# Kernel tuning notes

Hardware: AMD Instinct MI355X
Metric: run time of the kernel (lower is better)

Reference implementation:

```python
import jax, jax.numpy as jnp
import numpy as np

N_BINS = 1024
GAMMA = 0.99
BETA = 0.25
MIN_ASSIGN = 0.1 / N_BINS  # self.min_assignment
INITIAL_PATIENCE = 10.0


def setup_inputs() -> dict:
    key = jax.random.key(0)
    ks = jax.random.split(key, 5)
    N, d_x, d_z = 262144, 64, 32
    return {
        "x": jax.random.normal(ks[0], (N, d_x), jnp.float32),
        "W_enc": jax.random.normal(ks[1], (d_x, d_z), jnp.float32) / np.sqrt(d_x).astype(np.float32),
        "b_enc": jnp.zeros((d_z,), jnp.float32),
        "vectors": jax.random.normal(ks[2], (N_BINS, d_z), jnp.float32),
        "W_dec": jax.random.normal(ks[3], (d_z, d_x), jnp.float32) / np.sqrt(d_z).astype(np.float32),
        "b_dec": jnp.zeros((d_x,), jnp.float32),
        "assignments": jnp.full((N_BINS,), INITIAL_PATIENCE, jnp.float32),
        "noise": jax.random.normal(ks[4], (N_BINS, d_z), jnp.float32) * 1e-5,
    }


def _gauss_logprob(mu, x):
    # unit-variance Gaussian, summed over last (event) dim -> shape x.shape[:-1]
    d = x.shape[-1]
    return -0.5 * (jnp.sum((x - mu) ** 2, axis=-1) + d * jnp.log(2.0 * jnp.pi).astype(x.dtype))


def reference(x, W_enc, b_enc, vectors, W_dec, b_dec, assignments, noise):
    # ----- encoder + codebook nearest-neighbor lookup -----
    z = x @ W_enc + b_enc  # [N, d_z]
    # squared L2 distances to all codes: [N, n_bins]
    d2 = (jnp.sum(z * z, axis=-1, keepdims=True)
          - 2.0 * (z @ vectors.T)
          + jnp.sum(vectors * vectors, axis=-1)[None, :])
    idx = jnp.argmin(d2, axis=-1)          # [N]
    quantized = vectors[idx]               # [N, d_z]
    z_q = z + jax.lax.stop_gradient(quantized - z)  # straight-through

    # ----- reconstruction (Gaussian decoder) + commitment -----
    mu = z_q @ W_dec + b_dec
    reconstruction_loss = -jnp.mean(_gauss_logprob(mu, x))
    commitment_loss = jnp.mean((jax.lax.stop_gradient(quantized) - z) ** 2)
    loss = reconstruction_loss + BETA * commitment_loss

    # ----- training-mode buffer updates (EMA + dead-code reinit) -----
    N = idx.shape[0]
    # one_hot.mean(0) without materializing [N, n_bins]
    counts = jax.ops.segment_sum(jnp.ones((N,), jnp.float32), idx, num_segments=N_BINS)
    batch_assign = counts / N                                   # [n_bins]
    assign_ema = GAMMA * assignments + (1.0 - GAMMA) * batch_assign
    # (one_hot[:,:,None] * z[:,None,:]).sum(0) == per-bin sum of z
    sum_z = jax.ops.segment_sum(jax.lax.stop_gradient(z), idx, num_segments=N_BINS)
    mean_vector = sum_z / (batch_assign[:, None] * N)           # may be nan where count==0 (masked below)

    not_assigned = assign_ema * N < MIN_ASSIGN                  # [n_bins] bool
    max_idx = jnp.argmax(batch_assign)                          # constant through the loop (as in torch)

    def step(carry, i):
        vecs, a = carry
        do = not_assigned[i]
        new_a = a[max_idx] / 2.0
        vecs = vecs.at[i].set(jnp.where(do, vecs[max_idx] + noise[i], vecs[i]))
        a = a.at[i].set(jnp.where(do, new_a, a[i]))
        a = a.at[max_idx].set(jnp.where(do, new_a, a[max_idx]))
        return (vecs, a), None

    # torch pops from the end of the not-assigned list -> iterate high->low index
    (vecs2, assign_ema), _ = jax.lax.scan(step, (vectors, assign_ema),
                                          jnp.arange(N_BINS - 1, -1, -1))

    mean_vector = jnp.where(batch_assign[:, None] == 0.0, vecs2, mean_vector)
    new_vectors = GAMMA * vecs2 + (1.0 - GAMMA) * mean_vector
    return loss, new_vectors, assign_ema
```

## Files before the change

kernel.cpp:

```cpp
#include <hip/hip_runtime.h>
#include <math.h>

#define N_ROWS 262144
#define DX 64
#define DZ 32
#define NB 1024
#define NBF 262144.0f
#define MIN_ASSIGN (0.1f / 1024.0f)
#define BIAS 512.0f

typedef short shortx8 __attribute__((ext_vector_type(8)));
typedef float floatx4 __attribute__((ext_vector_type(4)));
typedef float floatx2 __attribute__((ext_vector_type(2)));

#define WS_RECON  0
#define WS_COMMIT 1
#define WS_VNORMB 64
#define WS_MUNORM 1088
#define WS_WENCT  2112
#define WS_WDECB  3136
#define WS_VBF    4160
#define WS_VBF2   20544
#define WS_ZP     36928
#define WS_BIDX   4231232
#define WS_SUMZC  4362304
#define WS_COUNTS 4395072
#define WS_PART   4396096
#define WS_FINS   6558784
#define WS_RPART  6559872
#define WS_CPART  6563968
#define WS_TOTAL  6568064
#define PART_STRIDE 33792
#define HCHUNKS 64
#define HROWS  (N_ROWS / HCHUNKS)
#define HROLES 17
#define HBLOCKS (HROLES * HCHUNKS)
#define HSCALE 2048.0f
#define RF_BLOCKS 132
#define ENC_THREADS 128
#define ENC_BLOCKS (N_ROWS / ENC_THREADS)

#define XSTR 68
#define ZSTR 40
#define YSTR 36
#define SMEM_ZBF  0
#define SMEM_YBF  10240
#define SMEM_XBF  0
#define SMEM_SKEY 19456
#define SMEM_SZ   19968

#define FB_RECON  0
#define FB_COMMIT 1
#define FB_COUNTS 64
#define FB_SUMZ   1088
#define FB_VNORM  33856
#define FB_MUTAB  34880
#define FB_ZERO_N 33856

static __device__ __forceinline__ short f2bf(float f) {
    union { float f; unsigned u; } v; v.f = f;
    unsigned r = v.u + 0x7FFFu + ((v.u >> 16) & 1u);
    return (short)(r >> 16);
}
static __device__ __forceinline__ float bits2f(unsigned u) {
    union { unsigned u; float f; } v; v.u = u; return v.f;
}

__global__ __launch_bounds__(256) void zero_kernel(float* __restrict__ p, int n) {
    int i = blockIdx.x * 256 + threadIdx.x;
    if (i < n) p[i] = 0.0f;
}

__global__ __launch_bounds__(64) void vq_prep(
    const float* __restrict__ vectors, const float* __restrict__ W_enc,
    const float* __restrict__ W_dec, const float* __restrict__ b_dec,
    float* __restrict__ ws)
{
    const int j = blockIdx.x;
    const int t = threadIdx.x;
    float* vnormb = ws + WS_VNORMB;
    float* munorm = ws + WS_MUNORM;
    short* vbf  = (short*)(ws + WS_VBF);
    short* vbf2 = (short*)(ws + WS_VBF2);
    short* wencT = (short*)(ws + WS_WENCT);
    short* wdecb = (short*)(ws + WS_WDECB);

    if (j == 0 && t == 2) ws[WS_FINS + 2] = 0.0f;
    if (j == 0) {
        #pragma unroll
        for (int c = 0; c < DZ; ++c)
            wencT[c * DX + t] = f2bf(W_enc[t * DZ + c]);
    }
    if (j == 1) {
        #pragma unroll
        for (int c = 0; c < DZ; ++c)
            wdecb[c * DX + t] = f2bf(W_dec[c * DX + t]);
    }

    __shared__ float v[DZ];
    if (t < DZ) {
        float vv = vectors[j * DZ + t];
        v[t] = vv;
        vbf[j * DZ + t]  = f2bf(vv);
        vbf2[j * DZ + t] = f2bf(-2.0f * vv);
    }
    __syncthreads();
    float m = b_dec[t];
    #pragma unroll
    for (int k = 0; k < DZ; ++k) m = fmaf(v[k], W_dec[k * DX + t], m);
    float ms = m * m;
    #pragma unroll
    for (int off = 32; off > 0; off >>= 1) ms += __shfl_down(ms, off, 64);
    if (t == 0) {
        munorm[j] = ms;
        float s = 0.0f;
        #pragma unroll
        for (int k = 0; k < DZ; ++k) s = fmaf(v[k], v[k], s);
        vnormb[j] = s + BIAS;
    }
}

__global__ __launch_bounds__(ENC_THREADS, 4) void vq_encmin(
    const float* __restrict__ x, const short* __restrict__ wencT,
    const float* __restrict__ b_enc, const short* __restrict__ wdecb,
    const float* __restrict__ b_dec, const short* __restrict__ vbf,
    const short* __restrict__ vbf2, const float* __restrict__ vnormb,
    const float* __restrict__ munorm,
    unsigned* __restrict__ zp, unsigned short* __restrict__ bidx_out,
    float* __restrict__ rpart, float* __restrict__ cpart)
{
    __shared__ __attribute__((aligned(16))) char smem[SMEM_SZ];
    short* xbf = (short*)(smem + SMEM_XBF);
    short* zbf = (short*)(smem + SMEM_ZBF);
    short* ybf = (short*)(smem + SMEM_YBF);
    unsigned* skey = (unsigned*)(smem + SMEM_SKEY);

    const int t = threadIdx.x;
    const int r = blockIdx.x * ENC_THREADS + t;

    const float4* xsrc = (const float4*)(x + (size_t)blockIdx.x * ENC_THREADS * DX);
    #pragma unroll
    for (int i = 0; i < 16; ++i) {
        float4 v = xsrc[i * ENC_THREADS + t];
        unsigned a0 = __builtin_bit_cast(unsigned, v.x) + 0x8000u;
        unsigned a1 = __builtin_bit_cast(unsigned, v.y) + 0x8000u;
        unsigned a2 = __builtin_bit_cast(unsigned, v.z) + 0x8000u;
        unsigned a3 = __builtin_bit_cast(unsigned, v.w) + 0x8000u;
        uint2 pv;
        pv.x = __builtin_amdgcn_perm(a1, a0, 0x07060302u);
        pv.y = __builtin_amdgcn_perm(a3, a2, 0x07060302u);
        const int e = i * ENC_THREADS + t;
        *(uint2*)&xbf[(e >> 4) * XSTR + (e & 15) * 4] = pv;
    }
    __syncthreads();

    float xnorm = 0.0f, xb = 0.0f;
    #pragma unroll
    for (int i = 0; i < 16; ++i) {
        uint2 q = *(const uint2*)&xbf[t * XSTR + i * 4];
        const float4 bd = ((const float4*)b_dec)[i];
        float f0 = bits2f(q.x << 16), f1 = bits2f(q.x & 0xFFFF0000u);
        float f2 = bits2f(q.y << 16), f3 = bits2f(q.y & 0xFFFF0000u);
        xnorm = fmaf(f0, f0, xnorm); xnorm = fmaf(f1, f1, xnorm);
        xnorm = fmaf(f2, f2, xnorm); xnorm = fmaf(f3, f3, xnorm);
        xb = fmaf(f0, bd.x, xb); xb = fmaf(f1, bd.y, xb);
        xb = fmaf(f2, bd.z, xb); xb = fmaf(f3, bd.w, xb);
    }

    const int w = t >> 6, l = t & 63, lm = l & 15, lq4 = l >> 4;
    shortx8 we[2][2], wd[2][2];
    #pragma unroll
    for (int ct = 0; ct < 2; ++ct)
        #pragma unroll
        for (int kk = 0; kk < 2; ++kk) {
            we[ct][kk] = *(const shortx8*)&wencT[(ct * 16 + lm) * DX + kk * 32 + lq4 * 8];
            wd[ct][kk] = *(const shortx8*)&wdecb[(ct * 16 + lm) * DX + kk * 32 + lq4 * 8];
        }
    const float be0 = b_enc[lm], be1 = b_enc[16 + lm];

    unsigned zpkv[16], ypkv[16];
    #pragma unroll
    for (int rt = 0; rt < 4; ++rt) {
        const int arow = (w * 64 + rt * 16 + lm) * XSTR;
        union { uint2 q[2]; shortx8 s; } a0u, a1u;
        a0u.q[0] = *(const uint2*)&xbf[arow + lq4 * 8];
        a0u.q[1] = *(const uint2*)&xbf[arow + lq4 * 8 + 4];
        a1u.q[0] = *(const uint2*)&xbf[arow + 32 + lq4 * 8];
        a1u.q[1] = *(const uint2*)&xbf[arow + 32 + lq4 * 8 + 4];

        floatx4 z0 = {be0, be0, be0, be0}, z1 = {be1, be1, be1, be1};
        z0 = __builtin_amdgcn_mfma_f32_16x16x32_bf16(a0u.s, we[0][0], z0, 0, 0, 0);
        z0 = __builtin_amdgcn_mfma_f32_16x16x32_bf16(a1u.s, we[0][1], z0, 0, 0, 0);
        z1 = __builtin_amdgcn_mfma_f32_16x16x32_bf16(a0u.s, we[1][0], z1, 0, 0, 0);
        z1 = __builtin_amdgcn_mfma_f32_16x16x32_bf16(a1u.s, we[1][1], z1, 0, 0, 0);
        floatx4 y0 = {0.f, 0.f, 0.f, 0.f}, y1 = {0.f, 0.f, 0.f, 0.f};
        y0 = __builtin_amdgcn_mfma_f32_16x16x32_bf16(a0u.s, wd[0][0], y0, 0, 0, 0);
        y0 = __builtin_amdgcn_mfma_f32_16x16x32_bf16(a1u.s, wd[0][1], y0, 0, 0, 0);
        y1 = __builtin_amdgcn_mfma_f32_16x16x32_bf16(a0u.s, wd[1][0], y1, 0, 0, 0);
        y1 = __builtin_amdgcn_mfma_f32_16x16x32_bf16(a1u.s, wd[1][1], y1, 0, 0, 0);

        #pragma unroll
        for (int reg = 0; reg < 4; ++reg) {
            unsigned zl = __builtin_bit_cast(unsigned, z0[reg]) + 0x8000u;
            unsigned zh = __builtin_bit_cast(unsigned, z1[reg]) + 0x8000u;
            zpkv[rt * 4 + reg] = __builtin_amdgcn_perm(zh, zl, 0x07060302u);
            unsigned yl = __builtin_bit_cast(unsigned, y0[reg]) + 0x8000u;
            unsigned yh = __builtin_bit_cast(unsigned, y1[reg]) + 0x8000u;
            ypkv[rt * 4 + reg] = __builtin_amdgcn_perm(yh, yl, 0x07060302u);
        }
    }
    __syncthreads();

    #pragma unroll
    for (int k = 0; k < 16; ++k) {
        const int row = w * 64 + (k >> 2) * 16 + lq4 * 4 + (k & 3);
        zbf[row * ZSTR + lm]      = (short)(zpkv[k] & 0xFFFFu);
        zbf[row * ZSTR + 16 + lm] = (short)(zpkv[k] >> 16);
        ybf[row * YSTR + lm]      = (short)(ypkv[k] & 0xFFFFu);
        ybf[row * YSTR + 16 + lm] = (short)(ypkv[k] >> 16);
    }
    __syncthreads();

    shortx8 afrag[4];
    #pragma unroll
    for (int rt = 0; rt < 4; ++rt)
        afrag[rt] = *(const shortx8*)&zbf[(w * 64 + rt * 16 + lm) * ZSTR + lq4 * 8];

    unsigned key[16];
    #pragma unroll
    for (int k = 0; k < 16; ++k) key[k] = 0xFFFFFFFFu;

    #pragma unroll 8
    for (int jt = 0; jt < 64; ++jt) {
        const int jbase = jt * 16 + lm;
        const shortx8 bfrag = *(const shortx8*)&vbf2[(size_t)jbase * DZ + lq4 * 8];
        const float vn = vnormb[jbase];
        floatx4 cin = {vn, vn, vn, vn};
        #pragma unroll
        for (int rt = 0; rt < 4; ++rt) {
            floatx4 acc = __builtin_amdgcn_mfma_f32_16x16x32_bf16(
                afrag[rt], bfrag, cin, 0, 0, 0);
            #pragma unroll
            for (int reg = 0; reg < 4; ++reg) {
                unsigned u = __builtin_bit_cast(unsigned, acc[reg]);
                unsigned pk = (u & 0xFFFFFC00u) | (unsigned)jbase;
                int k = rt * 4 + reg;
                key[k] = key[k] < pk ? key[k] : pk;
            }
        }
    }

    #pragma unroll
    for (int k = 0; k < 16; ++k) {
        unsigned kv = key[k];
        #pragma unroll
        for (int m = 1; m <= 8; m <<= 1) {
            unsigned ov = __shfl_xor(kv, m, 64);
            kv = ov < kv ? ov : kv;
        }
        if (lm == 0)
            skey[w * 64 + (k >> 2) * 16 + lq4 * 4 + (k & 3)] = kv;
    }
    __syncthreads();

    const unsigned kr = skey[t];
    const int bsel = (int)(kr & 1023u);
    const float score = bits2f(kr & 0xFFFFFC00u);
    bidx_out[r] = (unsigned short)bsel;

    float znorm = 0.0f;
    #pragma unroll
    for (int i = 0; i < 4; ++i) {
        uint4 q = *(const uint4*)&zbf[t * ZSTR + i * 8];
        zp[(size_t)(4 * i + 0) * N_ROWS + r] = q.x;
        zp[(size_t)(4 * i + 1) * N_ROWS + r] = q.y;
        zp[(size_t)(4 * i + 2) * N_ROWS + r] = q.z;
        zp[(size_t)(4 * i + 3) * N_ROWS + r] = q.w;
        float f0 = bits2f(q.x << 16), f1 = bits2f(q.x & 0xFFFF0000u);
        float f2 = bits2f(q.y << 16), f3 = bits2f(q.y & 0xFFFF0000u);
        float f4 = bits2f(q.z << 16), f5 = bits2f(q.z & 0xFFFF0000u);
        float f6 = bits2f(q.w << 16), f7 = bits2f(q.w & 0xFFFF0000u);
        znorm = fmaf(f0, f0, znorm); znorm = fmaf(f1, f1, znorm);
        znorm = fmaf(f2, f2, znorm); znorm = fmaf(f3, f3, znorm);
        znorm = fmaf(f4, f4, znorm); znorm = fmaf(f5, f5, znorm);
        znorm = fmaf(f6, f6, znorm); znorm = fmaf(f7, f7, znorm);
    }
    float commit = znorm + (score - BIAS);

    float dot = 0.0f;
    #pragma unroll
    for (int i = 0; i < 8; ++i) {
        uint2 yq = *(const uint2*)&ybf[t * YSTR + i * 4];
        uint2 vq = *(const uint2*)&vbf[(size_t)bsel * DZ + i * 4];
        dot = fmaf(bits2f(yq.x << 16), bits2f(vq.x << 16), dot);
        dot = fmaf(bits2f(yq.x & 0xFFFF0000u), bits2f(vq.x & 0xFFFF0000u), dot);
        dot = fmaf(bits2f(yq.y << 16), bits2f(vq.y << 16), dot);
        dot = fmaf(bits2f(yq.y & 0xFFFF0000u), bits2f(vq.y & 0xFFFF0000u), dot);
    }
    float rs = xnorm - 2.0f * (dot + xb) + munorm[bsel];

    #pragma unroll
    for (int off = 32; off > 0; off >>= 1) {
        rs     += __shfl_down(rs, off, 64);
        commit += __shfl_down(commit, off, 64);
    }
    if (l == 0) {
        rpart[blockIdx.x * 2 + w] = rs;
        cpart[blockIdx.x * 2 + w] = commit;
    }
}

__global__ __launch_bounds__(256) void vq_hist(
    const unsigned* __restrict__ zp, const unsigned short* __restrict__ bidx,
    float* __restrict__ part)
{
    __shared__ int h[2 * NB];
    const int t = threadIdx.x;
    const int ci    = blockIdx.x % HROLES;
    const int chunk = blockIdx.x / HROLES;

    #pragma unroll
    for (int i = 0; i < 8; ++i) h[t + 256 * i] = 0;
    __syncthreads();

    const int base = chunk * HROWS;
    if (ci < 16) {
        const unsigned* zc = zp + (size_t)ci * N_ROWS;
        #pragma unroll 4
        for (int i = 0; i < HROWS / 256; ++i) {
            int r = base + t + 256 * i;
            unsigned w = zc[r];
            int b = bidx[r];
            atomicAdd(&h[b],      __float2int_rn(bits2f(w << 16) * HSCALE));
            atomicAdd(&h[b + NB], __float2int_rn(bits2f(w & 0xFFFF0000u) * HSCALE));
        }
        __syncthreads();
        float* pp = part + (size_t)chunk * PART_STRIDE + (size_t)(2 * ci) * NB;
        #pragma unroll
        for (int i = 0; i < 8; ++i)
            pp[t + 256 * i] = (float)h[t + 256 * i] * (1.0f / HSCALE);
    } else {
        #pragma unroll 4
        for (int i = 0; i < HROWS / 256; ++i) {
            int r = base + t + 256 * i;
            atomicAdd(&h[bidx[r]], 1);
        }
        __syncthreads();
        float* pp = part + (size_t)chunk * PART_STRIDE + (size_t)32 * NB;
        #pragma unroll
        for (int i = 0; i < 4; ++i) pp[t + 256 * i] = (float)h[t + 256 * i];
    }
}

__global__ __launch_bounds__(256) void vq_redfin(
    const float* __restrict__ part, const float* __restrict__ assignments,
    float* __restrict__ ws, float* __restrict__ out)
{
    const int t = threadIdx.x;
    {
        const int o = blockIdx.x * 256 + t;
        float s = 0.0f;
        #pragma unroll 8
        for (int c = 0; c < HCHUNKS; ++c)
            s += part[(size_t)c * PART_STRIDE + o];
        (ws + WS_SUMZC)[o] = s;
    }
    __shared__ int sdone;
    __threadfence();
    __syncthreads();
    if (t == 0) {
        unsigned old = atomicAdd((unsigned*)ws + WS_FINS + 2, 1u);
        sdone = ((old % (unsigned)RF_BLOCKS) == (unsigned)(RF_BLOCKS - 1)) ? 1 : 0;
    }
    __syncthreads();
    if (!sdone) return;
    __threadfence();

    __shared__ float h[2048];
    __shared__ float sred[4], cred[4];
    __shared__ int s_mx;
    const float* counts = ws + WS_COUNTS;

    {
        const float* rp = ws + WS_RPART;
        const float* cp = ws + WS_CPART;
        float rsum = 0.0f, csum = 0.0f;
        #pragma unroll
        for (int i = 0; i < 16; ++i) {
            rsum += rp[t + 256 * i];
            csum += cp[t + 256 * i];
        }
        #pragma unroll
        for (int off = 32; off > 0; off >>= 1) {
            rsum += __shfl_down(rsum, off, 64);
            csum += __shfl_down(csum, off, 64);
        }
        if ((t & 63) == 0) { sred[t >> 6] = rsum; cred[t >> 6] = csum; }
    }

    float* af           = h;
    unsigned char* dd   = (unsigned char*)(h + 1024);
    int*   tsum         = (int*)(h + 1280);
    float* rv           = h + 1536;
    int*   ri           = (int*)(h + 1792);

    float cnt[4]; int dloc[4];
    float bestv = -1.0f; int besti = 0;
    #pragma unroll
    for (int u = 0; u < 4; ++u) {
        int b = 4 * t + u;
        float c = counts[b]; cnt[u] = c;
        float ba = c / NBF;
        float ae = 0.99f * assignments[b] + 0.01f * ba;
        af[b] = ae;
        int d = (ae * NBF < MIN_ASSIGN) ? 1 : 0;
        dd[b] = (unsigned char)d; dloc[u] = d;
        if (ba > bestv) { bestv = ba; besti = b; }
    }
    rv[t] = bestv; ri[t] = besti;
    __syncthreads();
    for (int s = 128; s > 0; s >>= 1) {
        if (t < s) {
            float ov = rv[t + s]; int oi = ri[t + s];
            if (ov > rv[t] || (ov == rv[t] && oi < ri[t])) { rv[t] = ov; ri[t] = oi; }
        }
        __syncthreads();
    }
    if (t == 0) s_mx = ri[0];
    __syncthreads();
    const int mx = s_mx;
    const float a0mx = af[mx];
    const int na_mx = dd[mx];

    tsum[t] = dloc[0] + dloc[1] + dloc[2] + dloc[3];
    __syncthreads();
    for (int off = 1; off < 256; off <<= 1) {
        int v2 = (t + off < 256) ? tsum[t + off] : 0;
        __syncthreads();
        tsum[t] += v2;
        __syncthreads();
    }
    const int K = tsum[0];
    const int Snext = (t < 255) ? tsum[t + 1] : 0;
    int suf[4];
    suf[3] = dloc[3]; suf[2] = dloc[2] + suf[3];
    suf[1] = dloc[1] + suf[2]; suf[0] = dloc[0] + suf[1];

    #pragma unroll
    for (int u = 0; u < 4; ++u) {
        int b = 4 * t + u;
        float av = af[b];
        int rank = suf[u] + Snext;
        int isd = dd[b];
        if (isd) av = ldexpf(a0mx, -rank);
        if (b == mx && K > 0) av = ldexpf(a0mx, -K);
        out[1 + NB * DZ + b] = av;
        ws[WS_FINS + 64 + b] = (float)isd;
    }
    if (t == 0) {
        ((int*)ws)[WS_FINS] = mx;
        ws[WS_FINS + 1] = (float)na_mx;
        float rtot = sred[0] + sred[1] + sred[2] + sred[3];
        float ctot = cred[0] + cred[1] + cred[2] + cred[3];
        float recon = 0.5f * (rtot / NBF) + 32.0f * 1.8378770664093453f;
        float commit = ctot / (NBF * (float)DZ);
        out[0] = recon + 0.25f * commit;
    }
}

__global__ __launch_bounds__(256) void vq_fin_vec(
    const float* __restrict__ vectors, const float* __restrict__ noise,
    const float* __restrict__ ws, float* __restrict__ out)
{
    const int idx = blockIdx.x * 256 + threadIdx.x;
    const int b = idx >> 5, c = idx & 31;
    const int mx = ((const int*)ws)[WS_FINS];
    const float na_mx = ws[WS_FINS + 1];
    const float isd = ws[WS_FINS + 64 + b];
    const float cnt = (ws + WS_COUNTS)[b];
    const float* sumzc = ws + WS_SUMZC;

    float v2 = vectors[b * DZ + c];
    if (isd != 0.0f) {
        const float mxn = (b < mx) ? na_mx : 0.0f;
        v2 = vectors[mx * DZ + c] + mxn * noise[mx * DZ + c] + noise[b * DZ + c];
    }
    float mean = (cnt == 0.0f) ? v2 : (sumzc[(size_t)c * NB + b] / cnt);
    out[1 + b * DZ + c] = 0.99f * v2 + 0.01f * mean;
}

__global__ __launch_bounds__(64) void vq_prep_fb(
    const float* __restrict__ vectors, const float* __restrict__ W_dec,
    const float* __restrict__ b_dec, float* __restrict__ vnorm,
    float* __restrict__ mu_table)
{
    const int j = blockIdx.x;
    const int t = threadIdx.x;
    __shared__ float v[DZ];
    if (t < DZ) v[t] = vectors[j * DZ + t];
    __syncthreads();
    float m = b_dec[t];
    #pragma unroll
    for (int k = 0; k < DZ; ++k) m = fmaf(v[k], W_dec[k * DX + t], m);
    mu_table[(size_t)j * DX + t] = m;
    if (t == 0) {
        float s = 0.0f;
        #pragma unroll
        for (int k = 0; k < DZ; ++k) s = fmaf(v[k], v[k], s);
        vnorm[j] = s;
    }
}

__global__ __launch_bounds__(256) void vq_main_atomic(
    const float* __restrict__ x, const float* __restrict__ W_enc,
    const float* __restrict__ b_enc, const float* __restrict__ vectors,
    const float* __restrict__ vnorm, const float* __restrict__ mu_table,
    float* __restrict__ counts, float* __restrict__ sum_z,
    float* __restrict__ recon_acc, float* __restrict__ commit_acc)
{
    const int r = blockIdx.x * 256 + threadIdx.x;
    float xr[DX];
    const float4* xp = reinterpret_cast<const float4*>(x + (size_t)r * DX);
    #pragma unroll
    for (int i = 0; i < DX / 4; ++i) {
        float4 v = xp[i];
        xr[4 * i + 0] = v.x; xr[4 * i + 1] = v.y;
        xr[4 * i + 2] = v.z; xr[4 * i + 3] = v.w;
    }
    float z[DZ];
    #pragma unroll
    for (int c = 0; c < DZ; ++c) z[c] = b_enc[c];
    #pragma unroll
    for (int k = 0; k < DX; ++k) {
        float xk = xr[k];
        #pragma unroll
        for (int c = 0; c < DZ; ++c) z[c] = fmaf(xk, W_enc[k * DZ + c], z[c]);
    }
    float znorm = 0.0f;
    #pragma unroll
    for (int c = 0; c < DZ; ++c) znorm = fmaf(z[c], z[c], znorm);
    float zm2[DZ];
    #pragma unroll
    for (int c = 0; c < DZ; ++c) zm2[c] = -2.0f * z[c];

    float best = 3.4e38f;
    int bi = 0;
    for (int j = 0; j < NB; ++j) {
        const float* vj = vectors + j * DZ;
        float s0 = vnorm[j], s1 = 0.0f, s2 = 0.0f, s3 = 0.0f;
        #pragma unroll
        for (int c = 0; c < DZ; c += 4) {
            s0 = fmaf(zm2[c + 0], vj[c + 0], s0);
            s1 = fmaf(zm2[c + 1], vj[c + 1], s1);
            s2 = fmaf(zm2[c + 2], vj[c + 2], s2);
            s3 = fmaf(zm2[c + 3], vj[c + 3], s3);
        }
        float s = (s0 + s1) + (s2 + s3);
        if (s < best) { best = s; bi = j; }
    }
    float commit_row = znorm + best;

    float rs = 0.0f;
    const float4* mup = reinterpret_cast<const float4*>(mu_table + (size_t)bi * DX);
    #pragma unroll
    for (int i = 0; i < DX / 4; ++i) {
        float4 m = mup[i];
        float d0 = xr[4 * i + 0] - m.x; rs = fmaf(d0, d0, rs);
        float d1 = xr[4 * i + 1] - m.y; rs = fmaf(d1, d1, rs);
        float d2 = xr[4 * i + 2] - m.z; rs = fmaf(d2, d2, rs);
        float d3 = xr[4 * i + 3] - m.w; rs = fmaf(d3, d3, rs);
    }
    atomicAdd(&counts[bi], 1.0f);
    #pragma unroll
    for (int c = 0; c < DZ; ++c)
        atomicAdd(&sum_z[(size_t)bi * DZ + c], -0.5f * zm2[c]);
    #pragma unroll
    for (int off = 32; off > 0; off >>= 1) {
        rs += __shfl_down(rs, off, 64);
        commit_row += __shfl_down(commit_row, off, 64);
    }
    if ((threadIdx.x & 63) == 0) {
        atomicAdd(recon_acc, rs);
        atomicAdd(commit_acc, commit_row);
    }
}

__global__ __launch_bounds__(1024) void vq_finalize_fb(
    const float* __restrict__ vectors, const float* __restrict__ assignments,
    const float* __restrict__ noise, const float* __restrict__ counts,
    const float* __restrict__ sum_z, const float* __restrict__ recon_acc,
    const float* __restrict__ commit_acc, float* __restrict__ out)
{
    __shared__ float a[NB];
    __shared__ unsigned char na[NB];
    __shared__ float rv[NB];
    __shared__ int ri[NB];
    __shared__ int s_max_idx;
    const int t = threadIdx.x;

    const float cnt = counts[t];
    const float ba = cnt / NBF;
    const float ae = 0.99f * assignments[t] + 0.01f * ba;
    a[t] = ae;
    na[t] = (ae * NBF < MIN_ASSIGN) ? 1 : 0;
    rv[t] = ba; ri[t] = t;
    __syncthreads();
    for (int s = NB / 2; s > 0; s >>= 1) {
        if (t < s) {
            float ov = rv[t + s]; int oi = ri[t + s];
            if (ov > rv[t] || (ov == rv[t] && oi < ri[t])) { rv[t] = ov; ri[t] = oi; }
        }
        __syncthreads();
    }
    if (t == 0) s_max_idx = ri[0];
    __syncthreads();
    const int mx = s_max_idx;
    if (t == 0) {
        for (int i = NB - 1; i >= 0; --i) {
            if (na[i]) { float v = 0.5f * a[mx]; a[i] = v; a[mx] = v; }
        }
    }
    __syncthreads();
    out[1 + NB * DZ + t] = a[t];
    const bool dead = (na[t] != 0);
    #pragma unroll
    for (int c = 0; c < DZ; ++c) {
        float v2 = dead ? (vectors[mx * DZ + c] + noise[t * DZ + c])
                        : vectors[t * DZ + c];
        float mean = (cnt == 0.0f) ? v2 : (sum_z[(size_t)t * DZ + c] / cnt);
        out[1 + t * DZ + c] = 0.99f * v2 + 0.01f * mean;
    }
    if (t == 0) {
        float recon = 0.5f * (recon_acc[0] / NBF) + 32.0f * 1.8378770664093453f;
        float commit = commit_acc[0] / (NBF * (float)DZ);
        out[0] = recon + 0.25f * commit;
    }
}

extern "C" void kernel_launch(void* const* d_in, const int* in_sizes, int n_in,
                              void* d_out, int out_size, void* d_ws, size_t ws_size,
                              hipStream_t stream)
{
    const float* x           = (const float*)d_in[0];
    const float* W_enc       = (const float*)d_in[1];
    const float* b_enc       = (const float*)d_in[2];
    const float* vectors     = (const float*)d_in[3];
    const float* W_dec       = (const float*)d_in[4];
    const float* b_dec       = (const float*)d_in[5];
    const float* assignments = (const float*)d_in[6];
    const float* noise       = (const float*)d_in[7];
    float* out = (float*)d_out;
    float* ws  = (float*)d_ws;

    if (ws_size >= (size_t)WS_TOTAL * sizeof(float)) {
        vq_prep<<<NB, 64, 0, stream>>>(vectors, W_enc, W_dec, b_dec, ws);
        vq_encmin<<<ENC_BLOCKS, ENC_THREADS, 0, stream>>>(x,
            (const short*)(ws + WS_WENCT), b_enc,
            (const short*)(ws + WS_WDECB), b_dec,
            (const short*)(ws + WS_VBF), (const short*)(ws + WS_VBF2),
            ws + WS_VNORMB, ws + WS_MUNORM,
            (unsigned*)(ws + WS_ZP), (unsigned short*)(ws + WS_BIDX),
            ws + WS_RPART, ws + WS_CPART);
        vq_hist<<<HBLOCKS, 256, 0, stream>>>(
            (const unsigned*)(ws + WS_ZP),
            (const unsigned short*)(ws + WS_BIDX),
            ws + WS_PART);
        vq_redfin<<<RF_BLOCKS, 256, 0, stream>>>(
            ws + WS_PART, assignments, ws, out);
        vq_fin_vec<<<(NB * DZ) / 256, 256, 0, stream>>>(vectors, noise, ws, out);
    } else {
        zero_kernel<<<(FB_ZERO_N + 255) / 256, 256, 0, stream>>>(ws, FB_ZERO_N);
        vq_prep_fb<<<NB, 64, 0, stream>>>(vectors, W_dec, b_dec,
            ws + FB_VNORM, ws + FB_MUTAB);
        vq_main_atomic<<<N_ROWS / 256, 256, 0, stream>>>(x, W_enc, b_enc, vectors,
            ws + FB_VNORM, ws + FB_MUTAB, ws + FB_COUNTS, ws + FB_SUMZ,
            ws + FB_RECON, ws + FB_COMMIT);
        vq_finalize_fb<<<1, NB, 0, stream>>>(vectors, assignments, noise,
            ws + FB_COUNTS, ws + FB_SUMZ, ws + FB_RECON, ws + FB_COMMIT, out);
    }
}
```

Baseline: 164.2 us.

## Fuse partial reduction and finalize into histogram kernel via last-block pattern

Drops the separate reduce/finalize kernel. The last histogram block to finish (detected with an atomic counter) now reduces the count partials and runs the assignment/dead-code finalize. The per-bin sum_z reduction over chunks moves into the final vector kernel, with its thread mapping changed so bins are contiguous. This saves one launch and the SUMZC round trip, but the count reduction runs serially in a single block and output writes become strided.

```diff
diff --git a/kernel.cpp b/kernel.cpp
--- a/kernel.cpp
+++ b/kernel.cpp
@@ -36,7 +36,6 @@
 #define HROLES 17
 #define HBLOCKS (HROLES * HCHUNKS)
 #define HSCALE 2048.0f
-#define RF_BLOCKS 132
 #define ENC_THREADS 128
 #define ENC_BLOCKS (N_ROWS / ENC_THREADS)
 
@@ -312,8 +311,10 @@
 
 __global__ __launch_bounds__(256) void vq_hist(
     const unsigned* __restrict__ zp, const unsigned short* __restrict__ bidx,
-    float* __restrict__ part)
-{
+    const float* __restrict__ assignments, float* __restrict__ ws,
+    float* __restrict__ out)
+{
+    float* part = ws + WS_PART;
     __shared__ int h[2 * NB];
     const int t = threadIdx.x;
     const int ci    = blockIdx.x % HROLES;
@@ -350,37 +351,31 @@
         #pragma unroll
         for (int i = 0; i < 4; ++i) pp[t + 256 * i] = (float)h[t + 256 * i];
     }
-}
-
-__global__ __launch_bounds__(256) void vq_redfin(
-    const float* __restrict__ part, const float* __restrict__ assignments,
-    float* __restrict__ ws, float* __restrict__ out)
-{
-    const int t = threadIdx.x;
-    {
-        const int o = blockIdx.x * 256 + t;
+
+    __shared__ int sdone;
+    __threadfence();
+    __syncthreads();
+    if (t == 0) {
+        unsigned old = atomicAdd((unsigned*)ws + WS_FINS + 2, 1u);
+        sdone = ((old % (unsigned)HBLOCKS) == (unsigned)(HBLOCKS - 1)) ? 1 : 0;
+    }
+    __syncthreads();
+    if (!sdone) return;
+    __threadfence();
+
+    __shared__ float cs[NB];
+    #pragma unroll
+    for (int i = 0; i < 4; ++i) {
+        const int b = i * 256 + t;
         float s = 0.0f;
         #pragma unroll 8
         for (int c = 0; c < HCHUNKS; ++c)
-            s += part[(size_t)c * PART_STRIDE + o];
-        (ws + WS_SUMZC)[o] = s;
-    }
-    __shared__ int sdone;
-    __threadfence();
-    __syncthreads();
-    if (t == 0) {
-        unsigned old = atomicAdd((unsigned*)ws + WS_FINS + 2, 1u);
-        sdone = ((old % (unsigned)RF_BLOCKS) == (unsigned)(RF_BLOCKS - 1)) ? 1 : 0;
-    }
-    __syncthreads();
-    if (!sdone) return;
-    __threadfence();
-
-    __shared__ float h[2048];
+            s += part[(size_t)c * PART_STRIDE + (size_t)32 * NB + b];
+        cs[b] = s;
+        (ws + WS_COUNTS)[b] = s;
+    }
+
     __shared__ float sred[4], cred[4];
-    __shared__ int s_mx;
-    const float* counts = ws + WS_COUNTS;
-
     {
         const float* rp = ws + WS_RPART;
         const float* cp = ws + WS_CPART;
@@ -397,19 +392,22 @@
         }
         if ((t & 63) == 0) { sred[t >> 6] = rsum; cred[t >> 6] = csum; }
     }
-
-    float* af           = h;
-    unsigned char* dd   = (unsigned char*)(h + 1024);
-    int*   tsum         = (int*)(h + 1280);
-    float* rv           = h + 1536;
-    int*   ri           = (int*)(h + 1792);
+    __syncthreads();
+
+    __shared__ float h2[2048];
+    __shared__ int s_mx;
+    float* af           = h2;
+    unsigned char* dd   = (unsigned char*)(h2 + 1024);
+    int*   tsum         = (int*)(h2 + 1280);
+    float* rv           = h2 + 1536;
+    int*   ri           = (int*)(h2 + 1792);
 
     float cnt[4]; int dloc[4];
     float bestv = -1.0f; int besti = 0;
     #pragma unroll
     for (int u = 0; u < 4; ++u) {
         int b = 4 * t + u;
-        float c = counts[b]; cnt[u] = c;
+        float c = cs[b]; cnt[u] = c;
         float ba = c / NBF;
         float ae = 0.99f * assignments[b] + 0.01f * ba;
         af[b] = ae;
@@ -468,24 +466,31 @@
     }
 }
 
-__global__ __launch_bounds__(256) void vq_fin_vec(
+__global__ __launch_bounds__(256) void vq_finvec2(
     const float* __restrict__ vectors, const float* __restrict__ noise,
     const float* __restrict__ ws, float* __restrict__ out)
 {
     const int idx = blockIdx.x * 256 + threadIdx.x;
-    const int b = idx >> 5, c = idx & 31;
+    const int b = idx & (NB - 1);
+    const int c = idx >> 10;
+    const float* part = ws + WS_PART;
+
+    float s = 0.0f;
+    #pragma unroll 8
+    for (int ch = 0; ch < HCHUNKS; ++ch)
+        s += part[(size_t)ch * PART_STRIDE + (size_t)c * NB + b];
+
     const int mx = ((const int*)ws)[WS_FINS];
     const float na_mx = ws[WS_FINS + 1];
     const float isd = ws[WS_FINS + 64 + b];
     const float cnt = (ws + WS_COUNTS)[b];
-    const float* sumzc = ws + WS_SUMZC;
 
     float v2 = vectors[b * DZ + c];
     if (isd != 0.0f) {
         const float mxn = (b < mx) ? na_mx : 0.0f;
         v2 = vectors[mx * DZ + c] + mxn * noise[mx * DZ + c] + noise[b * DZ + c];
     }
-    float mean = (cnt == 0.0f) ? v2 : (sumzc[(size_t)c * NB + b] / cnt);
+    float mean = (cnt == 0.0f) ? v2 : (s / cnt);
     out[1 + b * DZ + c] = 0.99f * v2 + 0.01f * mean;
 }
 
@@ -664,10 +669,8 @@
         vq_hist<<<HBLOCKS, 256, 0, stream>>>(
             (const unsigned*)(ws + WS_ZP),
             (const unsigned short*)(ws + WS_BIDX),
-            ws + WS_PART);
-        vq_redfin<<<RF_BLOCKS, 256, 0, stream>>>(
-            ws + WS_PART, assignments, ws, out);
-        vq_fin_vec<<<(NB * DZ) / 256, 256, 0, stream>>>(vectors, noise, ws, out);
+            assignments, ws, out);
+        vq_finvec2<<<(NB * DZ) / 256, 256, 0, stream>>>(vectors, noise, ws, out);
     } else {
         zero_kernel<<<(FB_ZERO_N + 255) / 256, 256, 0, stream>>>(ws, FB_ZERO_N);
         vq_prep_fb<<<NB, 64, 0, stream>>>(vectors, W_dec, b_dec,
```

New measurement: 268.5 us. +63.5%, slower.

## Shrink encmin blocks to 64 rows, load x directly into MFMA fragments, drop block syncs

Applied to the files above, without the earlier changes.

The encoder/argmin kernel now handles 64 rows per block instead of 128, with 32 rows per wave. It loads x from global memory straight into MFMA A-fragments instead of staging it in shared memory, and it computes the decoder dot product per lane using shuffles. This removes the x and y shared buffers and all __syncthreads, lowers register and LDS use so occupancy can rise (launch bounds go from 4 to 8), and doubles the number of blocks. The costs are that the codebook B-fragments are reloaded for half as many rows, the final per-row stage runs on only half the lanes, and the partial-sum arrays double in size.

```diff
diff --git a/kernel.cpp b/kernel.cpp
--- a/kernel.cpp
+++ b/kernel.cpp
@@ -11,10 +11,7 @@
 
 typedef short shortx8 __attribute__((ext_vector_type(8)));
 typedef float floatx4 __attribute__((ext_vector_type(4)));
-typedef float floatx2 __attribute__((ext_vector_type(2)));
-
-#define WS_RECON  0
-#define WS_COMMIT 1
+
 #define WS_VNORMB 64
 #define WS_MUNORM 1088
 #define WS_WENCT  2112
@@ -28,8 +25,8 @@
 #define WS_PART   4396096
 #define WS_FINS   6558784
 #define WS_RPART  6559872
-#define WS_CPART  6563968
-#define WS_TOTAL  6568064
+#define WS_CPART  6568064
+#define WS_TOTAL  6576256
 #define PART_STRIDE 33792
 #define HCHUNKS 64
 #define HROWS  (N_ROWS / HCHUNKS)
@@ -38,16 +35,9 @@
 #define HSCALE 2048.0f
 #define RF_BLOCKS 132
 #define ENC_THREADS 128
-#define ENC_BLOCKS (N_ROWS / ENC_THREADS)
-
-#define XSTR 68
+#define ENC_ROWS 64
+#define ENC_BLOCKS (N_ROWS / ENC_ROWS)
 #define ZSTR 40
-#define YSTR 36
-#define SMEM_ZBF  0
-#define SMEM_YBF  10240
-#define SMEM_XBF  0
-#define SMEM_SKEY 19456
-#define SMEM_SZ   19968
 
 #define FB_RECON  0
 #define FB_COMMIT 1
@@ -64,6 +54,11 @@
 }
 static __device__ __forceinline__ float bits2f(unsigned u) {
     union { unsigned u; float f; } v; v.u = u; return v.f;
+}
+static __device__ __forceinline__ unsigned pk2(float lo, float hi) {
+    unsigned a = __builtin_bit_cast(unsigned, lo) + 0x8000u;
+    unsigned b = __builtin_bit_cast(unsigned, hi) + 0x8000u;
+    return __builtin_amdgcn_perm(b, a, 0x07060302u);
 }
 
 __global__ __launch_bounds__(256) void zero_kernel(float* __restrict__ p, int n) {
@@ -120,7 +115,7 @@
     }
 }
 
-__global__ __launch_bounds__(ENC_THREADS, 4) void vq_encmin(
+__global__ __launch_bounds__(ENC_THREADS, 8) void vq_encmin(
     const float* __restrict__ x, const short* __restrict__ wencT,
     const float* __restrict__ b_enc, const short* __restrict__ wdecb,
     const float* __restrict__ b_dec, const short* __restrict__ vbf,
@@ -129,115 +124,97 @@
     unsigned* __restrict__ zp, unsigned short* __restrict__ bidx_out,
     float* __restrict__ rpart, float* __restrict__ cpart)
 {
-    __shared__ __attribute__((aligned(16))) char smem[SMEM_SZ];
-    short* xbf = (short*)(smem + SMEM_XBF);
-    short* zbf = (short*)(smem + SMEM_ZBF);
-    short* ybf = (short*)(smem + SMEM_YBF);
-    unsigned* skey = (unsigned*)(smem + SMEM_SKEY);
+    __shared__ __attribute__((aligned(16))) short zbf[ENC_ROWS * ZSTR];
+    __shared__ unsigned skey[ENC_ROWS];
+    __shared__ float sdot[ENC_ROWS];
 
     const int t = threadIdx.x;
-    const int r = blockIdx.x * ENC_THREADS + t;
-
-    const float4* xsrc = (const float4*)(x + (size_t)blockIdx.x * ENC_THREADS * DX);
-    #pragma unroll
-    for (int i = 0; i < 16; ++i) {
-        float4 v = xsrc[i * ENC_THREADS + t];
-        unsigned a0 = __builtin_bit_cast(unsigned, v.x) + 0x8000u;
-        unsigned a1 = __builtin_bit_cast(unsigned, v.y) + 0x8000u;
-        unsigned a2 = __builtin_bit_cast(unsigned, v.z) + 0x8000u;
-        unsigned a3 = __builtin_bit_cast(unsigned, v.w) + 0x8000u;
-        uint2 pv;
-        pv.x = __builtin_amdgcn_perm(a1, a0, 0x07060302u);
-        pv.y = __builtin_amdgcn_perm(a3, a2, 0x07060302u);
-        const int e = i * ENC_THREADS + t;
-        *(uint2*)&xbf[(e >> 4) * XSTR + (e & 15) * 4] = pv;
-    }
-    __syncthreads();
+    const int w = t >> 6, l = t & 63, lm = l & 15, lq4 = l >> 4;
+    const int wrow0 = w * 32;
+    const int rowbase = blockIdx.x * ENC_ROWS + wrow0;
+
+    const float be0 = b_enc[lm], be1 = b_enc[16 + lm];
+    const float4 bd0 = *(const float4*)(b_dec + lq4 * 8);
+    const float4 bd1 = *(const float4*)(b_dec + lq4 * 8 + 4);
+    const float4 bd2 = *(const float4*)(b_dec + 32 + lq4 * 8);
+    const float4 bd3 = *(const float4*)(b_dec + 32 + lq4 * 8 + 4);
 
     float xnorm = 0.0f, xb = 0.0f;
-    #pragma unroll
-    for (int i = 0; i < 16; ++i) {
-        uint2 q = *(const uint2*)&xbf[t * XSTR + i * 4];
-        const float4 bd = ((const float4*)b_dec)[i];
-        float f0 = bits2f(q.x << 16), f1 = bits2f(q.x & 0xFFFF0000u);
-        float f2 = bits2f(q.y << 16), f3 = bits2f(q.y & 0xFFFF0000u);
-        xnorm = fmaf(f0, f0, xnorm); xnorm = fmaf(f1, f1, xnorm);
-        xnorm = fmaf(f2, f2, xnorm); xnorm = fmaf(f3, f3, xnorm);
-        xb = fmaf(f0, bd.x, xb); xb = fmaf(f1, bd.y, xb);
-        xb = fmaf(f2, bd.z, xb); xb = fmaf(f3, bd.w, xb);
-    }
-
-    const int w = t >> 6, l = t & 63, lm = l & 15, lq4 = l >> 4;
-    shortx8 we[2][2], wd[2][2];
-    #pragma unroll
-    for (int ct = 0; ct < 2; ++ct)
-        #pragma unroll
-        for (int kk = 0; kk < 2; ++kk) {
-            we[ct][kk] = *(const shortx8*)&wencT[(ct * 16 + lm) * DX + kk * 32 + lq4 * 8];
-            wd[ct][kk] = *(const shortx8*)&wdecb[(ct * 16 + lm) * DX + kk * 32 + lq4 * 8];
-        }
-    const float be0 = b_enc[lm], be1 = b_enc[16 + lm];
-
-    unsigned zpkv[16], ypkv[16];
-    #pragma unroll
-    for (int rt = 0; rt < 4; ++rt) {
-        const int arow = (w * 64 + rt * 16 + lm) * XSTR;
-        union { uint2 q[2]; shortx8 s; } a0u, a1u;
-        a0u.q[0] = *(const uint2*)&xbf[arow + lq4 * 8];
-        a0u.q[1] = *(const uint2*)&xbf[arow + lq4 * 8 + 4];
-        a1u.q[0] = *(const uint2*)&xbf[arow + 32 + lq4 * 8];
-        a1u.q[1] = *(const uint2*)&xbf[arow + 32 + lq4 * 8 + 4];
+    unsigned ypkv[8];
+
+    #pragma unroll
+    for (int rt = 0; rt < 2; ++rt) {
+        const float* xr = x + (size_t)(rowbase + rt * 16 + lm) * DX + lq4 * 8;
+        const float4 v0 = *(const float4*)(xr);
+        const float4 v1 = *(const float4*)(xr + 4);
+        const float4 v2 = *(const float4*)(xr + 32);
+        const float4 v3 = *(const float4*)(xr + 36);
+
+        float pn = v0.x*v0.x + v0.y*v0.y + v0.z*v0.z + v0.w*v0.w
+                 + v1.x*v1.x + v1.y*v1.y + v1.z*v1.z + v1.w*v1.w
+                 + v2.x*v2.x + v2.y*v2.y + v2.z*v2.z + v2.w*v2.w
+                 + v3.x*v3.x + v3.y*v3.y + v3.z*v3.z + v3.w*v3.w;
+        float pb = v0.x*bd0.x + v0.y*bd0.y + v0.z*bd0.z + v0.w*bd0.w
+                 + v1.x*bd1.x + v1.y*bd1.y + v1.z*bd1.z + v1.w*bd1.w
+                 + v2.x*bd2.x + v2.y*bd2.y + v2.z*bd2.z + v2.w*bd2.w
+                 + v3.x*bd3.x + v3.y*bd3.y + v3.z*bd3.z + v3.w*bd3.w;
+        pn += __shfl_xor(pn, 16, 64); pn += __shfl_xor(pn, 32, 64);
+        pb += __shfl_xor(pb, 16, 64); pb += __shfl_xor(pb, 32, 64);
+        if (rt == lq4) { xnorm = pn; xb = pb; }
+
+        union { uint2 q[2]; shortx8 s; } ax0, ax1;
+        ax0.q[0] = (uint2){pk2(v0.x, v0.y), pk2(v0.z, v0.w)};
+        ax0.q[1] = (uint2){pk2(v1.x, v1.y), pk2(v1.z, v1.w)};
+        ax1.q[0] = (uint2){pk2(v2.x, v2.y), pk2(v2.z, v2.w)};
+        ax1.q[1] = (uint2){pk2(v3.x, v3.y), pk2(v3.z, v3.w)};
+
+        const shortx8 we00 = *(const shortx8*)&wencT[(0 * 16 + lm) * DX + 0 * 32 + lq4 * 8];
+        const shortx8 we01 = *(const shortx8*)&wencT[(0 * 16 + lm) * DX + 1 * 32 + lq4 * 8];
+        const shortx8 we10 = *(const shortx8*)&wencT[(1 * 16 + lm) * DX + 0 * 32 + lq4 * 8];
+        const shortx8 we11 = *(const shortx8*)&wencT[(1 * 16 + lm) * DX + 1 * 32 + lq4 * 8];
+        const shortx8 wd00 = *(const shortx8*)&wdecb[(0 * 16 + lm) * DX + 0 * 32 + lq4 * 8];
+        const shortx8 wd01 = *(const shortx8*)&wdecb[(0 * 16 + lm) * DX + 1 * 32 + lq4 * 8];
+        const shortx8 wd10 = *(const shortx8*)&wdecb[(1 * 16 + lm) * DX + 0 * 32 + lq4 * 8];
+        const shortx8 wd11 = *(const shortx8*)&wdecb[(1 * 16 + lm) * DX + 1 * 32 + lq4 * 8];
 
         floatx4 z0 = {be0, be0, be0, be0}, z1 = {be1, be1, be1, be1};
-        z0 = __builtin_amdgcn_mfma_f32_16x16x32_bf16(a0u.s, we[0][0], z0, 0, 0, 0);
-        z0 = __builtin_amdgcn_mfma_f32_16x16x32_bf16(a1u.s, we[0][1], z0, 0, 0, 0);
-        z1 = __builtin_amdgcn_mfma_f32_16x16x32_bf16(a0u.s, we[1][0], z1, 0, 0, 0);
-        z1 = __builtin_amdgcn_mfma_f32_16x16x32_bf16(a1u.s, we[1][1], z1, 0, 0, 0);
+        z0 = __builtin_amdgcn_mfma_f32_16x16x32_bf16(ax0.s, we00, z0, 0, 0, 0);
+        z0 = __builtin_amdgcn_mfma_f32_16x16x32_bf16(ax1.s, we01, z0, 0, 0, 0);
+        z1 = __builtin_amdgcn_mfma_f32_16x16x32_bf16(ax0.s, we10, z1, 0, 0, 0);
+        z1 = __builtin_amdgcn_mfma_f32_16x16x32_bf16(ax1.s, we11, z1, 0, 0, 0);
         floatx4 y0 = {0.f, 0.f, 0.f, 0.f}, y1 = {0.f, 0.f, 0.f, 0.f};
-        y0 = __builtin_amdgcn_mfma_f32_16x16x32_bf16(a0u.s, wd[0][0], y0, 0, 0, 0);
-        y0 = __builtin_amdgcn_mfma_f32_16x16x32_bf16(a1u.s, wd[0][1], y0, 0, 0, 0);
-        y1 = __builtin_amdgcn_mfma_f32_16x16x32_bf16(a0u.s, wd[1][0], y1, 0, 0, 0);
-        y1 = __builtin_amdgcn_mfma_f32_16x16x32_bf16(a1u.s, wd[1][1], y1, 0, 0, 0);
+        y0 = __builtin_amdgcn_mfma_f32_16x16x32_bf16(ax0.s, wd00, y0, 0, 0, 0);
+        y0 = __builtin_amdgcn_mfma_f32_16x16x32_bf16(ax1.s, wd01, y0, 0, 0, 0);
+        y1 = __builtin_amdgcn_mfma_f32_16x16x32_bf16(ax0.s, wd10, y1, 0, 0, 0);
+        y1 = __builtin_amdgcn_mfma_f32_16x16x32_bf16(ax1.s, wd11, y1, 0, 0, 0);
 
         #pragma unroll
         for (int reg = 0; reg < 4; ++reg) {
-            unsigned zl = __builtin_bit_cast(unsigned, z0[reg]) + 0x8000u;
-            unsigned zh = __builtin_bit_cast(unsigned, z1[reg]) + 0x8000u;
-            zpkv[rt * 4 + reg] = __builtin_amdgcn_perm(zh, zl, 0x07060302u);
-            unsigned yl = __builtin_bit_cast(unsigned, y0[reg]) + 0x8000u;
-            unsigned yh = __builtin_bit_cast(unsigned, y1[reg]) + 0x8000u;
-            ypkv[rt * 4 + reg] = __builtin_amdgcn_perm(yh, yl, 0x07060302u);
-        }
-    }
-    __syncthreads();
-
-    #pragma unroll
-    for (int k = 0; k < 16; ++k) {
-        const int row = w * 64 + (k >> 2) * 16 + lq4 * 4 + (k & 3);
-        zbf[row * ZSTR + lm]      = (short)(zpkv[k] & 0xFFFFu);
-        zbf[row * ZSTR + 16 + lm] = (short)(zpkv[k] >> 16);
-        ybf[row * YSTR + lm]      = (short)(ypkv[k] & 0xFFFFu);
-        ybf[row * YSTR + 16 + lm] = (short)(ypkv[k] >> 16);
-    }
-    __syncthreads();
-
-    shortx8 afrag[4];
-    #pragma unroll
-    for (int rt = 0; rt < 4; ++rt)
-        afrag[rt] = *(const shortx8*)&zbf[(w * 64 + rt * 16 + lm) * ZSTR + lq4 * 8];
-
-    unsigned key[16];
-    #pragma unroll
-    for (int k = 0; k < 16; ++k) key[k] = 0xFFFFFFFFu;
-
-    #pragma unroll 8
+            const int row = wrow0 + rt * 16 + lq4 * 4 + reg;
+            const unsigned zpk = pk2(z0[reg], z1[reg]);
+            zbf[row * ZSTR + lm]      = (short)(zpk & 0xFFFFu);
+            zbf[row * ZSTR + 16 + lm] = (short)(zpk >> 16);
+            ypkv[rt * 4 + reg] = pk2(y0[reg], y1[reg]);
+        }
+    }
+
+    shortx8 afrag[2];
+    #pragma unroll
+    for (int rt = 0; rt < 2; ++rt)
+        afrag[rt] = *(const shortx8*)&zbf[(wrow0 + rt * 16 + lm) * ZSTR + lq4 * 8];
+
+    unsigned key[8];
+    #pragma unroll
+    for (int k = 0; k < 8; ++k) key[k] = 0xFFFFFFFFu;
+
+    #pragma unroll 4
     for (int jt = 0; jt < 64; ++jt) {
         const int jbase = jt * 16 + lm;
         const shortx8 bfrag = *(const shortx8*)&vbf2[(size_t)jbase * DZ + lq4 * 8];
         const float vn = vnormb[jbase];
         floatx4 cin = {vn, vn, vn, vn};
         #pragma unroll
-        for (int rt = 0; rt < 4; ++rt) {
+        for (int rt = 0; rt < 2; ++rt) {
             floatx4 acc = __builtin_amdgcn_mfma_f32_16x16x32_bf16(
                 afrag[rt], bfrag, cin, 0, 0, 0);
             #pragma unroll
@@ -251,7 +228,7 @@
     }
 
     #pragma unroll
-    for (int k = 0; k < 16; ++k) {
+    for (int k = 0; k < 8; ++k) {
         unsigned kv = key[k];
         #pragma unroll
         for (int m = 1; m <= 8; m <<= 1) {
@@ -259,46 +236,54 @@
             kv = ov < kv ? ov : kv;
         }
         if (lm == 0)
-            skey[w * 64 + (k >> 2) * 16 + lq4 * 4 + (k & 3)] = kv;
-    }
-    __syncthreads();
-
-    const unsigned kr = skey[t];
-    const int bsel = (int)(kr & 1023u);
-    const float score = bits2f(kr & 0xFFFFFC00u);
-    bidx_out[r] = (unsigned short)bsel;
-
-    float znorm = 0.0f;
-    #pragma unroll
-    for (int i = 0; i < 4; ++i) {
-        uint4 q = *(const uint4*)&zbf[t * ZSTR + i * 8];
-        zp[(size_t)(4 * i + 0) * N_ROWS + r] = q.x;
-        zp[(size_t)(4 * i + 1) * N_ROWS + r] = q.y;
-        zp[(size_t)(4 * i + 2) * N_ROWS + r] = q.z;
-        zp[(size_t)(4 * i + 3) * N_ROWS + r] = q.w;
-        float f0 = bits2f(q.x << 16), f1 = bits2f(q.x & 0xFFFF0000u);
-        float f2 = bits2f(q.y << 16), f3 = bits2f(q.y & 0xFFFF0000u);
-        float f4 = bits2f(q.z << 16), f5 = bits2f(q.z & 0xFFFF0000u);
-        float f6 = bits2f(q.w << 16), f7 = bits2f(q.w & 0xFFFF0000u);
-        znorm = fmaf(f0, f0, znorm); znorm = fmaf(f1, f1, znorm);
-        znorm = fmaf(f2, f2, znorm); znorm = fmaf(f3, f3, znorm);
-        znorm = fmaf(f4, f4, znorm); znorm = fmaf(f5, f5, znorm);
-        znorm = fmaf(f6, f6, znorm); znorm = fmaf(f7, f7, znorm);
-    }
-    float commit = znorm + (score - BIAS);
-
-    float dot = 0.0f;
-    #pragma unroll
-    for (int i = 0; i < 8; ++i) {
-        uint2 yq = *(const uint2*)&ybf[t * YSTR + i * 4];
-        uint2 vq = *(const uint2*)&vbf[(size_t)bsel * DZ + i * 4];
-        dot = fmaf(bits2f(yq.x << 16), bits2f(vq.x << 16), dot);
-        dot = fmaf(bits2f(yq.x & 0xFFFF0000u), bits2f(vq.x & 0xFFFF0000u), dot);
-        dot = fmaf(bits2f(yq.y << 16), bits2f(vq.y << 16), dot);
-        dot = fmaf(bits2f(yq.y & 0xFFFF0000u), bits2f(vq.y & 0xFFFF0000u), dot);
-    }
-    float rs = xnorm - 2.0f * (dot + xb) + munorm[bsel];
-
+            skey[wrow0 + (k >> 2) * 16 + lq4 * 4 + (k & 3)] = kv;
+    }
+
+    #pragma unroll
+    for (int k = 0; k < 8; ++k) {
+        const int row = wrow0 + (k >> 2) * 16 + lq4 * 4 + (k & 3);
+        const unsigned bsel = skey[row] & 1023u;
+        const float vlo = bits2f(((unsigned)(unsigned short)vbf[bsel * DZ + lm]) << 16);
+        const float vhi = bits2f(((unsigned)(unsigned short)vbf[bsel * DZ + 16 + lm]) << 16);
+        const float ylo = bits2f(ypkv[k] << 16);
+        const float yhi = bits2f(ypkv[k] & 0xFFFF0000u);
+        float p = fmaf(yhi, vhi, ylo * vlo);
+        p += __shfl_xor(p, 1, 64);
+        p += __shfl_xor(p, 2, 64);
+        p += __shfl_xor(p, 4, 64);
+        p += __shfl_xor(p, 8, 64);
+        if (lm == 0) sdot[row] = p;
+    }
+
+    float rs = 0.0f, commit = 0.0f;
+    if (l < 32) {
+        const int rowb = wrow0 + l;
+        const int rabs = blockIdx.x * ENC_ROWS + rowb;
+        const unsigned kr = skey[rowb];
+        const int bsel = (int)(kr & 1023u);
+        const float score = bits2f(kr & 0xFFFFFC00u);
+        bidx_out[rabs] = (unsigned short)bsel;
+
+        float znorm = 0.0f;
+        #pragma unroll
+        for (int i = 0; i < 4; ++i) {
+            uint4 q = *(const uint4*)&zbf[rowb * ZSTR + i * 8];
+            zp[(size_t)(4 * i + 0) * N_ROWS + rabs] = q.x;
+            zp[(size_t)(4 * i + 1) * N_ROWS + rabs] = q.y;
+            zp[(size_t)(4 * i + 2) * N_ROWS + rabs] = q.z;
+            zp[(size_t)(4 * i + 3) * N_ROWS + rabs] = q.w;
+            float f0 = bits2f(q.x << 16), f1 = bits2f(q.x & 0xFFFF0000u);
+            float f2 = bits2f(q.y << 16), f3 = bits2f(q.y & 0xFFFF0000u);
+            float f4 = bits2f(q.z << 16), f5 = bits2f(q.z & 0xFFFF0000u);
+            float f6 = bits2f(q.w << 16), f7 = bits2f(q.w & 0xFFFF0000u);
+            znorm = fmaf(f0, f0, znorm); znorm = fmaf(f1, f1, znorm);
+            znorm = fmaf(f2, f2, znorm); znorm = fmaf(f3, f3, znorm);
+            znorm = fmaf(f4, f4, znorm); znorm = fmaf(f5, f5, znorm);
+            znorm = fmaf(f6, f6, znorm); znorm = fmaf(f7, f7, znorm);
+        }
+        commit = znorm + (score - BIAS);
+        rs = xnorm - 2.0f * (sdot[rowb] + xb) + munorm[bsel];
+    }
     #pragma unroll
     for (int off = 32; off > 0; off >>= 1) {
         rs     += __shfl_down(rs, off, 64);
@@ -386,7 +371,7 @@
         const float* cp = ws + WS_CPART;
         float rsum = 0.0f, csum = 0.0f;
         #pragma unroll
-        for (int i = 0; i < 16; ++i) {
+        for (int i = 0; i < 32; ++i) {
             rsum += rp[t + 256 * i];
             csum += cp[t + 256 * i];
         }
```

New measurement: 214.2 us. +30.4%, slower.
